# Kernel tuning notes

Measured on AMD Instinct MI355X. Metric: run time of the kernel, lower is better.

## Reference

```python
import jax, jax.numpy as jnp
import numpy as np

B, T = 2, 2048
V, D, H, HS, L = 32000, 512, 8, 64, 4
FF = 4 * D
EPS = 1e-5


def layer_norm(x, g, b):
    mu = jnp.mean(x, axis=-1, keepdims=True)
    var = jnp.mean((x - mu) ** 2, axis=-1, keepdims=True)
    return (x - mu) * jax.lax.rsqrt(var + EPS) * g + b


def setup_inputs() -> dict:
    key = jax.random.key(0)
    ks = iter(jax.random.split(key, 32))
    s = 0.02
    n = lambda shape: jax.random.normal(next(ks), shape, dtype=jnp.float32) * s
    inp = {
        "idx": jax.random.randint(next(ks), (B, T), 0, V),
        "targets": jax.random.randint(next(ks), (B, T), 0, V),
        "tok_emb": n((V, D)),
        "pos_emb": n((T, D)),
        "ln1_g": jnp.ones((L, D)), "ln1_b": jnp.zeros((L, D)),
        "Wq": n((L, H, D, HS)), "Wk": n((L, H, D, HS)), "Wv": n((L, H, D, HS)),
        "Wo": n((L, H * HS, D)), "bo": jnp.zeros((L, D)),
        "ln2_g": jnp.ones((L, D)), "ln2_b": jnp.zeros((L, D)),
        "W1": n((L, D, FF)), "b1": jnp.zeros((L, FF)),
        "W2": n((L, FF, D)), "b2": jnp.zeros((L, D)),
        "lnf_g": jnp.ones((D,)), "lnf_b": jnp.zeros((D,)),
        "Wout": n((D, V)), "bout": jnp.zeros((V,)),
    }
    return inp


def reference(idx, targets, tok_emb, pos_emb, ln1_g, ln1_b, Wq, Wk, Wv, Wo, bo,
              ln2_g, ln2_b, W1, b1, W2, b2, lnf_g, lnf_b, Wout, bout):
    x = tok_emb[idx] + pos_emb[None, :idx.shape[1], :]  # [B,T,D]
    causal = jnp.tril(jnp.ones((T, T), dtype=bool))
    scale = 1.0 / jnp.sqrt(jnp.float32(D))  # NOTE: source divides by sqrt(C)=sqrt(n_embeddings)
    for l in range(L):
        h = layer_norm(x, ln1_g[l], ln1_b[l])
        q = jnp.einsum('btd,hde->bhte', h, Wq[l])
        k = jnp.einsum('btd,hde->bhte', h, Wk[l])
        v = jnp.einsum('btd,hde->bhte', h, Wv[l])
        w = jnp.einsum('bhte,bhse->bhts', q, k) * scale
        w = jnp.where(causal[None, None], w, -jnp.inf)
        w = jax.nn.softmax(w, axis=-1)  # dropout is identity in eval
        attn = jnp.einsum('bhts,bhse->bhte', w, v)
        attn = attn.transpose(0, 2, 1, 3).reshape(x.shape[0], T, H * HS)
        x = x + attn @ Wo[l] + bo[l]
        h2 = layer_norm(x, ln2_g[l], ln2_b[l])
        x = x + jax.nn.relu(h2 @ W1[l] + b1[l]) @ W2[l] + b2[l]
    x = layer_norm(x, lnf_g, lnf_b)
    logits = x @ Wout + bout  # [B,T,V]
    logp = jax.nn.log_softmax(logits, axis=-1)
    tgt_logp = jnp.take_along_axis(logp, targets[..., None], axis=-1)[..., 0]
    loss = -jnp.mean(tgt_logp)
    return loss, logits
```

## Files before the change

kernel.cpp:

```cpp
#include <hip/hip_runtime.h>
#include <hip/hip_bf16.h>
#include <math.h>

#define TT 2048
#define BB 2
#define VV 32000
#define DD 512
#define HH 8
#define HSS 64
#define LL 4
#define FF_ 2048
#define NBLK_V (VV / 128)

using bf16x8 = __attribute__((ext_vector_type(8))) short;
using floatx4 = __attribute__((ext_vector_type(4))) float;

__device__ __forceinline__ ushort f2bf(float f) {
    __hip_bfloat16 b = __float2bfloat16(f);
    return *reinterpret_cast<ushort*>(&b);
}
__device__ __forceinline__ float bf2f(ushort u) {
    union { unsigned int i; float f; } x; x.i = ((unsigned int)u) << 16; return x.f;
}
__device__ __forceinline__ void gload16(const void* g, void* l) {
    __builtin_amdgcn_global_load_lds(
        (const __attribute__((address_space(1))) void*)g,
        (__attribute__((address_space(3))) void*)l, 16, 0, 0);
}

__global__ __launch_bounds__(64)
void embed_kernel(const int* __restrict__ idx, const float* __restrict__ tok,
                  const float* __restrict__ pos, float* __restrict__ x)
{
    int row = blockIdx.x;
    int t = row & (TT - 1);
    int tokid = idx[row];
    int lane = threadIdx.x;
    const float4* tp = (const float4*)(tok + (size_t)tokid * DD);
    const float4* pp = (const float4*)(pos + (size_t)t * DD);
    float4* xp = (float4*)(x + (size_t)row * DD);
    int i0 = lane * 2;
    float4 a = tp[i0],   b4 = pp[i0];
    float4 c = tp[i0+1], d4 = pp[i0+1];
    xp[i0]   = make_float4(a.x + b4.x, a.y + b4.y, a.z + b4.z, a.w + b4.w);
    xp[i0+1] = make_float4(c.x + d4.x, c.y + d4.y, c.z + d4.z, c.w + d4.w);
}

__global__ __launch_bounds__(256)
void ln_kernel(const float* __restrict__ x, const float* __restrict__ g,
               const float* __restrict__ b, ushort* __restrict__ out)
{
    int wave = threadIdx.x >> 6;
    int lane = threadIdx.x & 63;
    int row  = blockIdx.x * 4 + wave;
    const float* xr = x + (size_t)row * DD;
    float4 v0 = *(const float4*)(xr + lane * 8);
    float4 v1 = *(const float4*)(xr + lane * 8 + 4);
    float s = v0.x + v0.y + v0.z + v0.w + v1.x + v1.y + v1.z + v1.w;
    float q = v0.x*v0.x + v0.y*v0.y + v0.z*v0.z + v0.w*v0.w
            + v1.x*v1.x + v1.y*v1.y + v1.z*v1.z + v1.w*v1.w;
    #pragma unroll
    for (int off = 32; off; off >>= 1) {
        s += __shfl_xor(s, off);
        q += __shfl_xor(q, off);
    }
    float mu  = s * (1.0f / DD);
    float var = q * (1.0f / DD) - mu * mu;
    float rs  = rsqrtf(var + 1e-5f);
    float4 g0 = *(const float4*)(g + lane * 8);
    float4 g1 = *(const float4*)(g + lane * 8 + 4);
    float4 b0 = *(const float4*)(b + lane * 8);
    float4 b1 = *(const float4*)(b + lane * 8 + 4);
    union { ushort u[8]; uint4 v; } pk;
    pk.u[0] = f2bf((v0.x - mu) * rs * g0.x + b0.x);
    pk.u[1] = f2bf((v0.y - mu) * rs * g0.y + b0.y);
    pk.u[2] = f2bf((v0.z - mu) * rs * g0.z + b0.z);
    pk.u[3] = f2bf((v0.w - mu) * rs * g0.w + b0.w);
    pk.u[4] = f2bf((v1.x - mu) * rs * g1.x + b1.x);
    pk.u[5] = f2bf((v1.y - mu) * rs * g1.y + b1.y);
    pk.u[6] = f2bf((v1.z - mu) * rs * g1.z + b1.z);
    pk.u[7] = f2bf((v1.w - mu) * rs * g1.w + b1.w);
    *(uint4*)(out + (size_t)row * DD + lane * 8) = pk.v;
}

__global__ __launch_bounds__(256)
void transpose_cvt(const float* __restrict__ in, ushort* __restrict__ out,
                   int N, int K, long inStrideZ, long outStrideZ)
{
    __shared__ float t[64][65];
    in  += (size_t)blockIdx.z * inStrideZ;
    out += (size_t)blockIdx.z * outStrideZ;
    const int n0 = blockIdx.x * 64, k0 = blockIdx.y * 64;
    const int r = threadIdx.x >> 2;
    const int c = (threadIdx.x & 3) * 16;
    #pragma unroll
    for (int j = 0; j < 16; j += 4) {
        float4 v = *(const float4*)&in[(size_t)(k0 + r) * N + n0 + c + j];
        t[r][c + j + 0] = v.x; t[r][c + j + 1] = v.y;
        t[r][c + j + 2] = v.z; t[r][c + j + 3] = v.w;
    }
    __syncthreads();
    union { ushort u[8]; uint4 v; } pk;
    ushort* orow = out + (size_t)(n0 + r) * K + k0 + c;
    #pragma unroll
    for (int half = 0; half < 2; ++half) {
        #pragma unroll
        for (int j = 0; j < 8; ++j) pk.u[j] = f2bf(t[c + half * 8 + j][r]);
        *(uint4*)(orow + half * 8) = pk.v;
    }
}

__global__ __launch_bounds__(256)
void qkv_transpose(const float* __restrict__ Wq, const float* __restrict__ Wk,
                   const float* __restrict__ Wv, ushort* __restrict__ out)
{
    __shared__ float t[64][65];
    const int z = blockIdx.y;
    const int sel = z >> 5, l = (z >> 3) & 3, h = z & 7;
    const float* in = (sel == 0 ? Wq : sel == 1 ? Wk : Wv)
                      + (size_t)l * (HH * DD * HSS) + (size_t)h * (DD * HSS);
    ushort* ob = out + (size_t)l * (3 * DD * DD) + (size_t)sel * (DD * DD)
                     + (size_t)h * (HSS * DD);
    const int d0 = blockIdx.x * 64;
    const int r = threadIdx.x >> 2;
    const int c = (threadIdx.x & 3) * 16;
    #pragma unroll
    for (int j = 0; j < 16; j += 4) {
        float4 v = *(const float4*)&in[(size_t)(d0 + r) * HSS + c + j];
        t[r][c + j + 0] = v.x; t[r][c + j + 1] = v.y;
        t[r][c + j + 2] = v.z; t[r][c + j + 3] = v.w;
    }
    __syncthreads();
    union { ushort u[8]; uint4 v; } pk;
    ushort* orow = ob + (size_t)r * DD + d0 + c;
    #pragma unroll
    for (int half = 0; half < 2; ++half) {
        #pragma unroll
        for (int j = 0; j < 8; ++j) pk.u[j] = f2bf(t[c + half * 8 + j][r]);
        *(uint4*)(orow + half * 8) = pk.v;
    }
}

__global__ __launch_bounds__(256, 4)
void mfma_gemm(const ushort* __restrict__ A, int lda,
               const ushort* __restrict__ Bt, int ldb,
               float* __restrict__ Cf, ushort* __restrict__ Cbf, int ldc,
               const float* __restrict__ bias,
               const float* __restrict__ resid, int ldres,
               int K, int relu, int grp,
               float* __restrict__ smax, float* __restrict__ ssum, int nblks)
{
    __shared__ ushort As[16 * 512];
    __shared__ ushort Bs[16 * 512];
    __shared__ float sstat[2][128][2];

    int bxx = blockIdx.x, byy = blockIdx.y;
    if (grp > 0) {
        const int npm = gridDim.y, npn = gridDim.x;
        const int pid = blockIdx.y * npn + blockIdx.x;
        const int pig = grp * npn;
        const int gid = pid / pig;
        const int fm  = gid * grp;
        const int gsz = min(npm - fm, grp);
        byy = fm + (pid % gsz);
        bxx = (pid % pig) / gsz;
    }
    const int m0 = byy << 7, n0 = bxx << 7;
    const int tid = threadIdx.x, w = tid >> 6, lane = tid & 63;
    const int wm = w >> 1, wn = w & 1;
    const int l15 = lane & 15, lk = lane >> 4;

    floatx4 acc[4][4] = {};

    for (int k0 = 0; k0 < K; k0 += 64) {
        #pragma unroll
        for (int i = 0; i < 4; ++i) {
            int c = 4 * w + i;
            int cg = c >> 3, cmi = (c >> 1) & 3, ckh = c & 1;
            const ushort* ga = A + (size_t)(m0 + cg * 64 + cmi * 16 + l15) * lda
                                 + k0 + lk * 8 + ckh * 32;
            gload16(ga, &As[c * 512]);
            const ushort* gb = Bt + (size_t)(n0 + cg * 64 + cmi * 16 + l15) * ldb
                                  + k0 + lk * 8 + ckh * 32;
            gload16(gb, &Bs[c * 512]);
        }
        __syncthreads();
        #pragma unroll
        for (int kh = 0; kh < 2; ++kh) {
            bf16x8 af[4], bfr[4];
            #pragma unroll
            for (int mi = 0; mi < 4; ++mi)
                af[mi] = *(const bf16x8*)&As[((wm * 8 + mi * 2 + kh) * 64 + lane) * 8];
            #pragma unroll
            for (int ni = 0; ni < 4; ++ni)
                bfr[ni] = *(const bf16x8*)&Bs[((wn * 8 + ni * 2 + kh) * 64 + lane) * 8];
            #pragma unroll
            for (int mi = 0; mi < 4; ++mi)
                #pragma unroll
                for (int ni = 0; ni < 4; ++ni)
                    acc[mi][ni] = __builtin_amdgcn_mfma_f32_16x16x32_bf16(
                        af[mi], bfr[ni], acc[mi][ni], 0, 0, 0);
        }
        __syncthreads();
    }

    #pragma unroll
    for (int mi = 0; mi < 4; ++mi)
        #pragma unroll
        for (int ni = 0; ni < 4; ++ni)
            #pragma unroll
            for (int r = 0; r < 4; ++r) {
                float v = acc[mi][ni][r];
                if (bias) v += bias[n0 + wn * 64 + ni * 16 + l15];
                if (relu) v = fmaxf(v, 0.0f);
                acc[mi][ni][r] = v;
            }

    #pragma unroll
    for (int mi = 0; mi < 4; ++mi) {
        #pragma unroll
        for (int r = 0; r < 4; ++r) {
            int grow = m0 + wm * 64 + mi * 16 + lk * 4 + r;
            #pragma unroll
            for (int ni = 0; ni < 4; ++ni) {
                int gcol = n0 + wn * 64 + ni * 16 + l15;
                float v = acc[mi][ni][r];
                if (resid) v += resid[(size_t)grow * ldres + gcol];
                if (Cbf) Cbf[(size_t)grow * ldc + gcol] = f2bf(v);
                else     Cf [(size_t)grow * ldc + gcol] = v;
            }
        }
    }

    if (smax) {
        #pragma unroll
        for (int mi = 0; mi < 4; ++mi) {
            #pragma unroll
            for (int r = 0; r < 4; ++r) {
                float m4 = fmaxf(fmaxf(acc[mi][0][r], acc[mi][1][r]),
                                 fmaxf(acc[mi][2][r], acc[mi][3][r]));
                m4 = fmaxf(m4, __shfl_xor(m4, 1));
                m4 = fmaxf(m4, __shfl_xor(m4, 2));
                m4 = fmaxf(m4, __shfl_xor(m4, 4));
                m4 = fmaxf(m4, __shfl_xor(m4, 8));
                float s4 = 0.f;
                #pragma unroll
                for (int ni = 0; ni < 4; ++ni) s4 += __expf(acc[mi][ni][r] - m4);
                s4 += __shfl_xor(s4, 1);
                s4 += __shfl_xor(s4, 2);
                s4 += __shfl_xor(s4, 4);
                s4 += __shfl_xor(s4, 8);
                if (l15 == 0) {
                    int R = wm * 64 + mi * 16 + lk * 4 + r;
                    sstat[0][R][wn] = m4;
                    sstat[1][R][wn] = s4;
                }
            }
        }
        __syncthreads();
        if (tid < 128) {
            float ma = sstat[0][tid][0], mb = sstat[0][tid][1];
            float M = fmaxf(ma, mb);
            float S = sstat[1][tid][0] * __expf(ma - M)
                    + sstat[1][tid][1] * __expf(mb - M);
            smax[(size_t)(m0 + tid) * nblks + bxx] = M;
            ssum[(size_t)(m0 + tid) * nblks + bxx] = S;
        }
    }
}

__global__ __launch_bounds__(256, 2)
void mfma_gemm_db(const ushort* __restrict__ A, int lda,
                  const ushort* __restrict__ Bt, int ldb,
                  float* __restrict__ Cf, ushort* __restrict__ Cbf, int ldc,
                  const float* __restrict__ bias,
                  const float* __restrict__ resid, int ldres,
                  int K, int relu)
{
    __shared__ ushort st[2][2][8192];

    const int m0 = blockIdx.y << 7, n0 = blockIdx.x << 7;
    const int tid = threadIdx.x, w = tid >> 6, lane = tid & 63;
    const int wm = w >> 1, wn = w & 1;
    const int l15 = lane & 15, lk = lane >> 4;
    const int nt = K >> 6;

    auto STAGE = [&](int t, int p) {
        const int k0 = t << 6;
        #pragma unroll
        for (int i = 0; i < 4; ++i) {
            int c = 4 * w + i;
            int cg = c >> 3, cmi = (c >> 1) & 3, ckh = c & 1;
            gload16(A + (size_t)(m0 + cg * 64 + cmi * 16 + l15) * lda
                      + k0 + lk * 8 + ckh * 32, &st[p][0][c * 512]);
            gload16(Bt + (size_t)(n0 + cg * 64 + cmi * 16 + l15) * ldb
                       + k0 + lk * 8 + ckh * 32, &st[p][1][c * 512]);
        }
    };

    floatx4 acc[4][4] = {};
    STAGE(0, 0);

    for (int t = 0; t < nt; ++t) {
        const int p = t & 1;
        if (t + 1 < nt) {
            STAGE(t + 1, p ^ 1);
            asm volatile("s_waitcnt vmcnt(8)" ::: "memory");
        } else {
            asm volatile("s_waitcnt vmcnt(0)" ::: "memory");
        }
        __builtin_amdgcn_s_barrier();
        __builtin_amdgcn_sched_barrier(0);
        #pragma unroll
        for (int kh = 0; kh < 2; ++kh) {
            bf16x8 af[4], bfr[4];
            #pragma unroll
            for (int mi = 0; mi < 4; ++mi)
                af[mi] = *(const bf16x8*)&st[p][0][((wm * 8 + mi * 2 + kh) * 64 + lane) * 8];
            #pragma unroll
            for (int ni = 0; ni < 4; ++ni)
                bfr[ni] = *(const bf16x8*)&st[p][1][((wn * 8 + ni * 2 + kh) * 64 + lane) * 8];
            #pragma unroll
            for (int mi = 0; mi < 4; ++mi)
                #pragma unroll
                for (int ni = 0; ni < 4; ++ni)
                    acc[mi][ni] = __builtin_amdgcn_mfma_f32_16x16x32_bf16(
                        af[mi], bfr[ni], acc[mi][ni], 0, 0, 0);
        }
        __builtin_amdgcn_sched_barrier(0);
        __builtin_amdgcn_s_barrier();
    }

    #pragma unroll
    for (int mi = 0; mi < 4; ++mi)
        #pragma unroll
        for (int ni = 0; ni < 4; ++ni)
            #pragma unroll
            for (int r = 0; r < 4; ++r) {
                float v = acc[mi][ni][r];
                if (bias) v += bias[n0 + wn * 64 + ni * 16 + l15];
                if (relu) v = fmaxf(v, 0.0f);
                acc[mi][ni][r] = v;
            }

    #pragma unroll
    for (int mi = 0; mi < 4; ++mi) {
        #pragma unroll
        for (int r = 0; r < 4; ++r) {
            int grow = m0 + wm * 64 + mi * 16 + lk * 4 + r;
            #pragma unroll
            for (int ni = 0; ni < 4; ++ni) {
                int gcol = n0 + wn * 64 + ni * 16 + l15;
                float v = acc[mi][ni][r];
                if (resid) v += resid[(size_t)grow * ldres + gcol];
                if (Cbf) Cbf[(size_t)grow * ldc + gcol] = f2bf(v);
                else     Cf [(size_t)grow * ldc + gcol] = v;
            }
        }
    }
}

__global__ __launch_bounds__(256)
void attn_mfma_kernel(const ushort* __restrict__ qkv, ushort* __restrict__ out)
{
    __shared__ ushort Vt[64][72];
    __shared__ ushort Pl[64][72];

    const int z = blockIdx.y, b = z >> 3, h = z & 7;
    const int q0 = blockIdx.x << 6;
    const int tid = threadIdx.x;
    const int w = tid >> 6, lane = tid & 63;
    const int l15 = lane & 15, g = lane >> 4;
    const float scale = 0.04419417382415922f;

    const int vkey = tid & 63, vd0 = (tid >> 6) * 16;

    bf16x8 qf0, qf1;
    {
        const ushort* qp = qkv + ((size_t)(b * TT + q0 + 16 * w + l15)) * 1536
                               + h * HSS + g * 8;
        qf0 = *(const bf16x8*)qp;
        qf1 = *(const bf16x8*)(qp + 32);
    }

    floatx4 acc_o[4] = {};
    float lreg[4] = {};

    for (int s0 = 0; s0 <= q0; s0 += 64) {
        __syncthreads();
        {
            const ushort* vp = qkv + ((size_t)(b * TT + s0 + vkey)) * 1536
                                   + 1024 + h * HSS + vd0;
            bf16x8 v0 = *(const bf16x8*)vp;
            bf16x8 v1 = *(const bf16x8*)(vp + 8);
            #pragma unroll
            for (int j = 0; j < 8; ++j) {
                Vt[vd0 + j][vkey]     = (ushort)v0[j];
                Vt[vd0 + 8 + j][vkey] = (ushort)v1[j];
            }
        }

        floatx4 s4[4] = {};
        #pragma unroll
        for (int kb = 0; kb < 4; ++kb) {
            const ushort* kp = qkv + ((size_t)(b * TT + s0 + kb * 16 + l15)) * 1536
                                   + 512 + h * HSS + g * 8;
            bf16x8 kf0 = *(const bf16x8*)kp;
            bf16x8 kf1 = *(const bf16x8*)(kp + 32);
            s4[kb] = __builtin_amdgcn_mfma_f32_16x16x32_bf16(qf0, kf0, s4[kb], 0, 0, 0);
            s4[kb] = __builtin_amdgcn_mfma_f32_16x16x32_bf16(qf1, kf1, s4[kb], 0, 0, 0);
        }

        const bool diag = (s0 == q0);
        #pragma unroll
        for (int r = 0; r < 4; ++r) {
            const int qrow = q0 + 16 * w + g * 4 + r;
            #pragma unroll
            for (int kb = 0; kb < 4; ++kb) {
                float xs = s4[kb][r] * scale;
                if (diag && (s0 + kb * 16 + l15) > qrow) xs = -1e30f;
                float p = __expf(xs);
                lreg[r] += p;
                Pl[16 * w + g * 4 + r][kb * 16 + l15] = f2bf(p);
            }
        }
        __syncthreads();

        bf16x8 pa0 = *(const bf16x8*)&Pl[16 * w + l15][g * 8];
        bf16x8 pa1 = *(const bf16x8*)&Pl[16 * w + l15][g * 8 + 32];
        #pragma unroll
        for (int db = 0; db < 4; ++db) {
            bf16x8 vb0 = *(const bf16x8*)&Vt[db * 16 + l15][g * 8];
            bf16x8 vb1 = *(const bf16x8*)&Vt[db * 16 + l15][g * 8 + 32];
            acc_o[db] = __builtin_amdgcn_mfma_f32_16x16x32_bf16(pa0, vb0, acc_o[db], 0, 0, 0);
            acc_o[db] = __builtin_amdgcn_mfma_f32_16x16x32_bf16(pa1, vb1, acc_o[db], 0, 0, 0);
        }
    }

    #pragma unroll
    for (int r = 0; r < 4; ++r) {
        float l = lreg[r];
        l += __shfl_xor(l, 1);
        l += __shfl_xor(l, 2);
        l += __shfl_xor(l, 4);
        l += __shfl_xor(l, 8);
        float inv = 1.0f / l;
        ushort* op = out + ((size_t)(b * TT + q0 + 16 * w + g * 4 + r)) * DD + h * HSS;
        #pragma unroll
        for (int db = 0; db < 4; ++db)
            op[db * 16 + l15] = f2bf(acc_o[db][r] * inv);
    }
}

__global__ __launch_bounds__(256)
void rowloss_finalize(const float* __restrict__ logits, const int* __restrict__ targets,
                      const float* __restrict__ smax, const float* __restrict__ ssum,
                      float* __restrict__ rowloss)
{
    const int wv = threadIdx.x >> 6, lane = threadIdx.x & 63;
    const int row = blockIdx.x * 4 + wv;
    const float* mrow = smax + (size_t)row * NBLK_V;
    const float* srow = ssum + (size_t)row * NBLK_V;
    float M = -1e30f;
    for (int i = lane; i < NBLK_V; i += 64) M = fmaxf(M, mrow[i]);
    #pragma unroll
    for (int off = 32; off; off >>= 1) M = fmaxf(M, __shfl_xor(M, off));
    float S = 0.f;
    for (int i = lane; i < NBLK_V; i += 64) S += srow[i] * __expf(mrow[i] - M);
    #pragma unroll
    for (int off = 32; off; off >>= 1) S += __shfl_xor(S, off);
    if (lane == 0)
        rowloss[row] = -(logits[(size_t)row * VV + targets[row]] - M - logf(S));
}

__global__ __launch_bounds__(256)
void loss_finalize(const float* __restrict__ rowloss, float* __restrict__ out)
{
    __shared__ float red[256];
    float s = 0.f;
    for (int i = threadIdx.x; i < BB * TT; i += 256) s += rowloss[i];
    red[threadIdx.x] = s; __syncthreads();
    for (int s2 = 128; s2; s2 >>= 1) {
        if (threadIdx.x < s2) red[threadIdx.x] += red[threadIdx.x + s2];
        __syncthreads();
    }
    if (threadIdx.x == 0) out[0] = red[0] * (1.0f / (BB * TT));
}

extern "C" void kernel_launch(void* const* d_in, const int* in_sizes, int n_in,
                              void* d_out, int out_size, void* d_ws, size_t ws_size,
                              hipStream_t stream) {
    const int*   idx     = (const int*)  d_in[0];
    const int*   targets = (const int*)  d_in[1];
    const float* tok_emb = (const float*)d_in[2];
    const float* pos_emb = (const float*)d_in[3];
    const float* ln1_g   = (const float*)d_in[4];
    const float* ln1_b   = (const float*)d_in[5];
    const float* Wq      = (const float*)d_in[6];
    const float* Wk      = (const float*)d_in[7];
    const float* Wv      = (const float*)d_in[8];
    const float* Wo      = (const float*)d_in[9];
    const float* bo      = (const float*)d_in[10];
    const float* ln2_g   = (const float*)d_in[11];
    const float* ln2_b   = (const float*)d_in[12];
    const float* W1      = (const float*)d_in[13];
    const float* b1      = (const float*)d_in[14];
    const float* W2      = (const float*)d_in[15];
    const float* b2      = (const float*)d_in[16];
    const float* lnf_g   = (const float*)d_in[17];
    const float* lnf_b   = (const float*)d_in[18];
    const float* Wout    = (const float*)d_in[19];
    const float* bout    = (const float*)d_in[20];

    float* outf   = (float*)d_out;
    float* logits = outf + 1;

    const size_t ROW = (size_t)BB * TT;

    float*  x     = (float*)d_ws;
    ushort* h_bf  = (ushort*)(x + ROW * DD);
    ushort* Woutt = h_bf + ROW * DD;
    float*  rowloss = (float*)(Woutt + (size_t)VV * DD);
    float* smax = x;
    float* ssum = x + ROW * NBLK_V;

    ushort* sc     = (ushort*)(outf + 8);
    ushort* qkv_bf = sc;
    ushort* ff_bf  = qkv_bf + ROW * 1536;
    ushort* Wqkvt  = ff_bf + ROW * FF_;
    ushort* Wot    = Wqkvt + (size_t)LL * 1536 * DD;
    ushort* W1t    = Wot   + (size_t)LL * DD * DD;
    ushort* W2t    = W1t   + (size_t)LL * FF_ * DD;

    qkv_transpose<<<dim3(8, 96), 256, 0, stream>>>(Wq, Wk, Wv, Wqkvt);
    transpose_cvt<<<dim3(8, 8, LL),  256, 0, stream>>>(Wo,   Wot,   DD,  DD,  (long)DD*DD,   (long)DD*DD);
    transpose_cvt<<<dim3(32, 8, LL), 256, 0, stream>>>(W1,   W1t,   FF_, DD,  (long)DD*FF_,  (long)DD*FF_);
    transpose_cvt<<<dim3(8, 32, LL), 256, 0, stream>>>(W2,   W2t,   DD,  FF_, (long)FF_*DD,  (long)FF_*DD);
    transpose_cvt<<<dim3(500, 8, 1), 256, 0, stream>>>(Wout, Woutt, VV,  DD,  0, 0);

    embed_kernel<<<ROW, 64, 0, stream>>>(idx, tok_emb, pos_emb, x);

    for (int l = 0; l < LL; ++l) {
        ln_kernel<<<ROW / 4, 256, 0, stream>>>(x, ln1_g + l * DD, ln1_b + l * DD, h_bf);

        mfma_gemm_db<<<dim3(1536 / 128, ROW / 128), 256, 0, stream>>>(
            h_bf, DD, Wqkvt + (size_t)l * 1536 * DD, DD,
            nullptr, qkv_bf, 1536, nullptr, nullptr, 0, DD, 0);

        attn_mfma_kernel<<<dim3(TT / 64, BB * HH), 256, 0, stream>>>(qkv_bf, h_bf);

        mfma_gemm_db<<<dim3(DD / 128, ROW / 128), 256, 0, stream>>>(
            h_bf, DD, Wot + (size_t)l * DD * DD, DD,
            x, nullptr, DD, bo + l * DD, x, DD, DD, 0);

        ln_kernel<<<ROW / 4, 256, 0, stream>>>(x, ln2_g + l * DD, ln2_b + l * DD, h_bf);

        mfma_gemm_db<<<dim3(FF_ / 128, ROW / 128), 256, 0, stream>>>(
            h_bf, DD, W1t + (size_t)l * FF_ * DD, DD,
            nullptr, ff_bf, FF_, b1 + l * FF_, nullptr, 0, DD, 1);

        mfma_gemm_db<<<dim3(DD / 128, ROW / 128), 256, 0, stream>>>(
            ff_bf, FF_, W2t + (size_t)l * DD * FF_, FF_,
            x, nullptr, DD, b2 + l * DD, x, DD, FF_, 0);
    }

    ln_kernel<<<ROW / 4, 256, 0, stream>>>(x, lnf_g, lnf_b, h_bf);

    mfma_gemm<<<dim3(VV / 128, ROW / 128), 256, 0, stream>>>(
        h_bf, DD, Woutt, DD,
        logits, nullptr, VV, bout, nullptr, 0, DD, 0, 8,
        smax, ssum, NBLK_V);

    rowloss_finalize<<<ROW / 4, 256, 0, stream>>>(logits, targets, smax, ssum, rowloss);
    loss_finalize<<<1, 256, 0, stream>>>(rowloss, outf);
}
```

Before: 1.404 ms.

## Specialize logits GEMM with 256x128 tiles and 512-thread blocks

Replaces the generic GEMM used for the vocabulary projection with a dedicated kernel that uses 512 threads and 256-row by 128-column tiles, so each B (Wout) tile loaded into shared memory is reused by twice as many rows. The grouped block-index swizzle and the runtime branches for resid, relu and bf16 output are removed. The per-block online-softmax statistics are widened to 256 rows. The larger tile raises LDS use and register pressure per block, and dropping the swizzle may change L2 reuse of the A and Wout tiles.

```diff
diff --git a/kernel.cpp b/kernel.cpp
--- a/kernel.cpp
+++ b/kernel.cpp
@@ -141,31 +141,20 @@
     }
 }
 
-__global__ __launch_bounds__(256, 4)
-void mfma_gemm(const ushort* __restrict__ A, int lda,
-               const ushort* __restrict__ Bt, int ldb,
-               float* __restrict__ Cf, ushort* __restrict__ Cbf, int ldc,
-               const float* __restrict__ bias,
-               const float* __restrict__ resid, int ldres,
-               int K, int relu, int grp,
-               float* __restrict__ smax, float* __restrict__ ssum, int nblks)
-{
-    __shared__ ushort As[16 * 512];
+__global__ __launch_bounds__(512, 6)
+void mfma_gemm_logits(const ushort* __restrict__ A, int lda,
+                      const ushort* __restrict__ Bt, int ldb,
+                      float* __restrict__ Cf, int ldc,
+                      const float* __restrict__ bias,
+                      int K,
+                      float* __restrict__ smax, float* __restrict__ ssum, int nblks)
+{
+    __shared__ ushort As[32 * 512];
     __shared__ ushort Bs[16 * 512];
-    __shared__ float sstat[2][128][2];
-
-    int bxx = blockIdx.x, byy = blockIdx.y;
-    if (grp > 0) {
-        const int npm = gridDim.y, npn = gridDim.x;
-        const int pid = blockIdx.y * npn + blockIdx.x;
-        const int pig = grp * npn;
-        const int gid = pid / pig;
-        const int fm  = gid * grp;
-        const int gsz = min(npm - fm, grp);
-        byy = fm + (pid % gsz);
-        bxx = (pid % pig) / gsz;
-    }
-    const int m0 = byy << 7, n0 = bxx << 7;
+    __shared__ float sstat[2][256][2];
+
+    const int bxx = blockIdx.x, byy = blockIdx.y;
+    const int m0 = byy << 8, n0 = bxx << 7;
     const int tid = threadIdx.x, w = tid >> 6, lane = tid & 63;
     const int wm = w >> 1, wn = w & 1;
     const int l15 = lane & 15, lk = lane >> 4;
@@ -176,13 +165,16 @@
         #pragma unroll
         for (int i = 0; i < 4; ++i) {
             int c = 4 * w + i;
-            int cg = c >> 3, cmi = (c >> 1) & 3, ckh = c & 1;
-            const ushort* ga = A + (size_t)(m0 + cg * 64 + cmi * 16 + l15) * lda
-                                 + k0 + lk * 8 + ckh * 32;
-            gload16(ga, &As[c * 512]);
-            const ushort* gb = Bt + (size_t)(n0 + cg * 64 + cmi * 16 + l15) * ldb
-                                  + k0 + lk * 8 + ckh * 32;
-            gload16(gb, &Bs[c * 512]);
+            int cg = c >> 1, ckh = c & 1;
+            gload16(A + (size_t)(m0 + cg * 16 + l15) * lda + k0 + lk * 8 + ckh * 32,
+                    &As[c * 512]);
+        }
+        #pragma unroll
+        for (int i = 0; i < 2; ++i) {
+            int c = 2 * w + i;
+            int cg = c >> 1, ckh = c & 1;
+            gload16(Bt + (size_t)(n0 + cg * 16 + l15) * ldb + k0 + lk * 8 + ckh * 32,
+                    &Bs[c * 512]);
         }
         __syncthreads();
         #pragma unroll
@@ -190,10 +182,10 @@
             bf16x8 af[4], bfr[4];
             #pragma unroll
             for (int mi = 0; mi < 4; ++mi)
-                af[mi] = *(const bf16x8*)&As[((wm * 8 + mi * 2 + kh) * 64 + lane) * 8];
+                af[mi] = *(const bf16x8*)&As[(((wm * 4 + mi) * 2 + kh) * 64 + lane) * 8];
             #pragma unroll
             for (int ni = 0; ni < 4; ++ni)
-                bfr[ni] = *(const bf16x8*)&Bs[((wn * 8 + ni * 2 + kh) * 64 + lane) * 8];
+                bfr[ni] = *(const bf16x8*)&Bs[(((wn * 4 + ni) * 2 + kh) * 64 + lane) * 8];
             #pragma unroll
             for (int mi = 0; mi < 4; ++mi)
                 #pragma unroll
@@ -207,14 +199,11 @@
     #pragma unroll
     for (int mi = 0; mi < 4; ++mi)
         #pragma unroll
-        for (int ni = 0; ni < 4; ++ni)
-            #pragma unroll
-            for (int r = 0; r < 4; ++r) {
-                float v = acc[mi][ni][r];
-                if (bias) v += bias[n0 + wn * 64 + ni * 16 + l15];
-                if (relu) v = fmaxf(v, 0.0f);
-                acc[mi][ni][r] = v;
-            }
+        for (int ni = 0; ni < 4; ++ni) {
+            float bv = bias[n0 + wn * 64 + ni * 16 + l15];
+            #pragma unroll
+            for (int r = 0; r < 4; ++r) acc[mi][ni][r] += bv;
+        }
 
     #pragma unroll
     for (int mi = 0; mi < 4; ++mi) {
@@ -222,50 +211,43 @@
         for (int r = 0; r < 4; ++r) {
             int grow = m0 + wm * 64 + mi * 16 + lk * 4 + r;
             #pragma unroll
-            for (int ni = 0; ni < 4; ++ni) {
-                int gcol = n0 + wn * 64 + ni * 16 + l15;
-                float v = acc[mi][ni][r];
-                if (resid) v += resid[(size_t)grow * ldres + gcol];
-                if (Cbf) Cbf[(size_t)grow * ldc + gcol] = f2bf(v);
-                else     Cf [(size_t)grow * ldc + gcol] = v;
+            for (int ni = 0; ni < 4; ++ni)
+                Cf[(size_t)grow * ldc + n0 + wn * 64 + ni * 16 + l15] = acc[mi][ni][r];
+        }
+    }
+
+    #pragma unroll
+    for (int mi = 0; mi < 4; ++mi) {
+        #pragma unroll
+        for (int r = 0; r < 4; ++r) {
+            float m4 = fmaxf(fmaxf(acc[mi][0][r], acc[mi][1][r]),
+                             fmaxf(acc[mi][2][r], acc[mi][3][r]));
+            m4 = fmaxf(m4, __shfl_xor(m4, 1));
+            m4 = fmaxf(m4, __shfl_xor(m4, 2));
+            m4 = fmaxf(m4, __shfl_xor(m4, 4));
+            m4 = fmaxf(m4, __shfl_xor(m4, 8));
+            float s4 = 0.f;
+            #pragma unroll
+            for (int ni = 0; ni < 4; ++ni) s4 += __expf(acc[mi][ni][r] - m4);
+            s4 += __shfl_xor(s4, 1);
+            s4 += __shfl_xor(s4, 2);
+            s4 += __shfl_xor(s4, 4);
+            s4 += __shfl_xor(s4, 8);
+            if (l15 == 0) {
+                int R = wm * 64 + mi * 16 + lk * 4 + r;
+                sstat[0][R][wn] = m4;
+                sstat[1][R][wn] = s4;
             }
         }
     }
-
-    if (smax) {
-        #pragma unroll
-        for (int mi = 0; mi < 4; ++mi) {
-            #pragma unroll
-            for (int r = 0; r < 4; ++r) {
-                float m4 = fmaxf(fmaxf(acc[mi][0][r], acc[mi][1][r]),
-                                 fmaxf(acc[mi][2][r], acc[mi][3][r]));
-                m4 = fmaxf(m4, __shfl_xor(m4, 1));
-                m4 = fmaxf(m4, __shfl_xor(m4, 2));
-                m4 = fmaxf(m4, __shfl_xor(m4, 4));
-                m4 = fmaxf(m4, __shfl_xor(m4, 8));
-                float s4 = 0.f;
-                #pragma unroll
-                for (int ni = 0; ni < 4; ++ni) s4 += __expf(acc[mi][ni][r] - m4);
-                s4 += __shfl_xor(s4, 1);
-                s4 += __shfl_xor(s4, 2);
-                s4 += __shfl_xor(s4, 4);
-                s4 += __shfl_xor(s4, 8);
-                if (l15 == 0) {
-                    int R = wm * 64 + mi * 16 + lk * 4 + r;
-                    sstat[0][R][wn] = m4;
-                    sstat[1][R][wn] = s4;
-                }
-            }
-        }
-        __syncthreads();
-        if (tid < 128) {
-            float ma = sstat[0][tid][0], mb = sstat[0][tid][1];
-            float M = fmaxf(ma, mb);
-            float S = sstat[1][tid][0] * __expf(ma - M)
-                    + sstat[1][tid][1] * __expf(mb - M);
-            smax[(size_t)(m0 + tid) * nblks + bxx] = M;
-            ssum[(size_t)(m0 + tid) * nblks + bxx] = S;
-        }
+    __syncthreads();
+    if (tid < 256) {
+        float ma = sstat[0][tid][0], mb = sstat[0][tid][1];
+        float M = fmaxf(ma, mb);
+        float S = sstat[1][tid][0] * __expf(ma - M)
+                + sstat[1][tid][1] * __expf(mb - M);
+        smax[(size_t)(m0 + tid) * nblks + bxx] = M;
+        ssum[(size_t)(m0 + tid) * nblks + bxx] = S;
     }
 }
 
@@ -566,9 +548,9 @@
 
     ln_kernel<<<ROW / 4, 256, 0, stream>>>(x, lnf_g, lnf_b, h_bf);
 
-    mfma_gemm<<<dim3(VV / 128, ROW / 128), 256, 0, stream>>>(
+    mfma_gemm_logits<<<dim3(VV / 128, ROW / 256), 512, 0, stream>>>(
         h_bf, DD, Woutt, DD,
-        logits, nullptr, VV, bout, nullptr, 0, DD, 0, 8,
+        logits, VV, bout, DD,
         smax, ssum, NBLK_V);
 
     rowloss_finalize<<<ROW / 4, 256, 0, stream>>>(logits, targets, smax, ssum, rowloss);
```

Result: slower. 2.232 ms (+59.0%).
